# Optimization experiments

Hardware: AMD Instinct MI355X
Metric: run time of the kernel (lower is better)

## Reference

```python
import jax, jax.numpy as jnp
import numpy as np

N, F_IN, H, C, E = 100000, 128, 128, 40, 600000


def setup_inputs() -> dict:
    key = jax.random.key(0)
    ks = jax.random.split(key, 20)
    s = 0.05
    inp = {
        "x": jax.random.normal(ks[0], (N, F_IN), jnp.float32),
        "edge_index": jax.random.randint(ks[1], (2, E), 0, N, jnp.int64),
        "importance": jnp.ones((F_IN,), jnp.float32),
        "W1": jax.random.normal(ks[2], (H, F_IN), jnp.float32) * s,
        "bl1": jax.random.normal(ks[3], (H,), jnp.float32) * s,
        "bc1": jnp.zeros((H,), jnp.float32),
        "W2": jax.random.normal(ks[4], (H, H), jnp.float32) * s,
        "bl2": jax.random.normal(ks[5], (H,), jnp.float32) * s,
        "bc2": jnp.zeros((H,), jnp.float32),
        "W3": jax.random.normal(ks[6], (H, H), jnp.float32) * s,
        "bl3": jax.random.normal(ks[7], (H,), jnp.float32) * s,
        "bc3": jnp.zeros((H,), jnp.float32),
        "Wlin1": jax.random.normal(ks[8], (H, H), jnp.float32) * s,
        "blin1": jax.random.normal(ks[9], (H,), jnp.float32) * s,
        "Wlin2": jax.random.normal(ks[10], (C, H), jnp.float32) * s,
        "blin2": jax.random.normal(ks[11], (C,), jnp.float32) * s,
    }
    return inp


def balanced_conv(x, W, bl, bc, row, col):
    # lin, then symmetric-normalized message, mean-aggregated over targets
    n = x.shape[0]
    h = x @ W.T + bl                                   # [N, H]
    loops = jnp.arange(n)
    r = jnp.concatenate([row, loops])                  # sources (x_j index)
    c = jnp.concatenate([col, loops])                  # targets
    deg = jnp.zeros((n,), x.dtype).at[c].add(1.0)      # degree(col) incl. self-loops
    dinv = deg ** -0.5
    norm = dinv[r] * dinv[c]                           # [E+N]
    msg = norm[:, None] * h[r]                         # gather + scale
    agg = jnp.zeros((n, h.shape[1]), x.dtype).at[c].add(msg)  # scatter-add
    return agg / deg[:, None] + bc                     # mean aggr + bias


def reference(x, edge_index, importance, W1, bl1, bc1, W2, bl2, bc2,
              W3, bl3, bc3, Wlin1, blin1, Wlin2, blin2):
    row, col = edge_index[0], edge_index[1]
    h = x * importance
    h = jax.nn.relu(balanced_conv(h, W1, bl1, bc1, row, col))
    h = jax.nn.relu(balanced_conv(h, W2, bl2, bc2, row, col))
    h = jax.nn.relu(balanced_conv(h, W3, bl3, bc3, row, col))
    h = jax.nn.relu(h @ Wlin1.T + blin1)
    h = h @ Wlin2.T + blin2
    return jax.nn.log_softmax(h, axis=-1)
```

## Files before the change

### kernel.cpp

```cpp
#include <hip/hip_runtime.h>
#include <hip/hip_bf16.h>

#define F 128
#define C_CLS 40
#define NWSPLIT 35
#define ELLCAP 32
#define NBKT 9

typedef __attribute__((ext_vector_type(8))) short short8;
typedef __attribute__((ext_vector_type(4))) float float4v;
typedef unsigned short ushort;

__device__ inline float bf2f(ushort u) {
  unsigned int x = ((unsigned int)u) << 16;
  return __builtin_bit_cast(float, x);
}
__device__ inline ushort f2bf(float f) {
  __hip_bfloat16 h = __float2bfloat16(f);
  return __builtin_bit_cast(ushort, h);
}
__device__ inline void split_bf16(float f, ushort& hi, ushort& lo) {
  hi = f2bf(f);
  lo = f2bf(f - bf2f(hi));
}
__device__ inline int swz(int lane) { return lane ^ ((lane >> 4) & 3); }
__device__ inline int bucket_of(int cv) {
  int lim = cv < ELLCAP ? cv : ELLCAP;
  int nIt = (lim + 3) >> 2;
  return 8 - nIt;
}

__global__ __launch_bounds__(256) void setup_kernel(
    const float* __restrict__ W1, const float* __restrict__ imp,
    const float* __restrict__ W2, const float* __restrict__ W3,
    const float* __restrict__ Wl1, const float* __restrict__ Wh2,
    ushort* __restrict__ WhP,
    ushort* __restrict__ W2hH, ushort* __restrict__ W2lH,
    const int* __restrict__ row, const int* __restrict__ col,
    int* __restrict__ cnt, int* __restrict__ ell,
    int ne, int n) {
  int b = blockIdx.x;
  if (b < NWSPLIT) {
    int ci = b * 256 + threadIdx.x;
    if (ci < 8192) {
      const float* src[4] = {W1, W2, W3, Wl1};
      int p = ci >> 11, c = ci & 2047;
      int kc = c >> 10, ct = (c >> 7) & 7, ks = (c >> 6) & 1, ln = c & 63;
      int dl = swz(ln);
      int colw = ct * 16 + (dl & 15);
      int k = kc * 64 + ks * 32 + (dl >> 4) * 8;
      float4 f0 = *(const float4*)&src[p][(size_t)colw * F + k];
      float4 f1 = *(const float4*)&src[p][(size_t)colw * F + k + 4];
      float v[8] = {f0.x, f0.y, f0.z, f0.w, f1.x, f1.y, f1.z, f1.w};
      if (p == 0) {
        float4 i0 = *(const float4*)&imp[k];
        float4 i1 = *(const float4*)&imp[k + 4];
        v[0] *= i0.x; v[1] *= i0.y; v[2] *= i0.z; v[3] *= i0.w;
        v[4] *= i1.x; v[5] *= i1.y; v[6] *= i1.z; v[7] *= i1.w;
      }
      ushort hi[8];
#pragma unroll
      for (int j = 0; j < 8; ++j) hi[j] = f2bf(v[j]);
      *(short8*)&WhP[(size_t)ci * 8] = *(short8*)hi;
    } else if (ci < 8192 + 768) {
      int c = ci - 8192;
      int ct = c >> 8, ks = (c >> 6) & 3, ln = c & 63;
      int colw = ct * 16 + (ln & 15);
      int k = ks * 32 + (ln >> 4) * 8;
      float v[8];
      if (colw < C_CLS) {
        float4 f0 = *(const float4*)&Wh2[(size_t)colw * F + k];
        float4 f1 = *(const float4*)&Wh2[(size_t)colw * F + k + 4];
        v[0] = f0.x; v[1] = f0.y; v[2] = f0.z; v[3] = f0.w;
        v[4] = f1.x; v[5] = f1.y; v[6] = f1.z; v[7] = f1.w;
      } else {
#pragma unroll
        for (int j = 0; j < 8; ++j) v[j] = 0.f;
      }
      ushort hi[8], lo[8];
#pragma unroll
      for (int j = 0; j < 8; ++j) split_bf16(v[j], hi[j], lo[j]);
      *(short8*)&W2hH[(size_t)c * 8] = *(short8*)hi;
      *(short8*)&W2lH[(size_t)c * 8] = *(short8*)lo;
    }
  } else {
    int e = (b - NWSPLIT) * 256 + threadIdx.x;
    if (e < ne) {
      int r = row[e], c = col[e];
      int p = atomicAdd(&cnt[c], 1);
      if (p < ELLCAP) ell[(size_t)c * ELLCAP + p] = r;
    }
  }
}

__global__ __launch_bounds__(256) void prepass_kernel(
    const float* __restrict__ x, const int* __restrict__ cnt,
    int* __restrict__ ell, float* __restrict__ wsum, int* __restrict__ hist,
    ushort* __restrict__ Xs, ushort* __restrict__ Az,
    int n, int nbW, int nbX) {
  int b = blockIdx.x;
  if (b < nbW) {
    __shared__ int lh[NBKT];
    int t = threadIdx.x;
    if (t < NBKT) lh[t] = 0;
    __syncthreads();
    int node = b * 256 + t;
    if (node < n) {
      int cv = cnt[node];
      int lim = cv < ELLCAP ? cv : ELLCAP;
      int lim4 = (lim + 3) & ~3;
      float gs = 0.f;
      const int4* ep = (const int4*)&ell[(size_t)node * ELLCAP];
      for (int base = 0; base < lim; base += 4) {
        int4 rr = ep[base >> 2];
        bool p1 = base + 1 < lim, p2 = base + 2 < lim, p3 = base + 3 < lim;
        int r1 = p1 ? rr.y : rr.x;
        int r2 = p2 ? rr.z : rr.x;
        int r3 = p3 ? rr.w : rr.x;
        float g0 = rsqrtf((float)(cnt[rr.x] + 1));
        float g1 = p1 ? rsqrtf((float)(cnt[r1] + 1)) : 0.f;
        float g2 = p2 ? rsqrtf((float)(cnt[r2] + 1)) : 0.f;
        float g3 = p3 ? rsqrtf((float)(cnt[r3] + 1)) : 0.f;
        gs += (g0 + g1) + (g2 + g3);
      }
      float d = (float)(cv + 1);
      wsum[node] = rsqrtf(d) * gs + 1.0f / d;
      for (int p = lim; p < lim4; ++p) ell[(size_t)node * ELLCAP + p] = n;
      atomicAdd(&lh[bucket_of(cv)], 1);
    }
    __syncthreads();
    if (t < NBKT) atomicAdd(&hist[t], lh[t]);
  } else if (b < nbW + nbX) {
    size_t i = (size_t)(b - nbW) * 2048 + (size_t)threadIdx.x * 8;
    if (i < (size_t)n * F) {
      int node = (int)(i >> 7);
      float dc = rsqrtf((float)(cnt[node] + 1));
      float4 f0 = *(const float4*)&x[i];
      float4 f1 = *(const float4*)&x[i + 4];
      ushort o[8] = {f2bf(dc * f0.x), f2bf(dc * f0.y), f2bf(dc * f0.z), f2bf(dc * f0.w),
                     f2bf(dc * f1.x), f2bf(dc * f1.y), f2bf(dc * f1.z), f2bf(dc * f1.w)};
      *(short8*)&Xs[i] = *(short8*)o;
    }
  } else {
    int t = threadIdx.x;
    short8 z = (short8){0, 0, 0, 0, 0, 0, 0, 0};
    if (t < 16) *(short8*)&Xs[(size_t)n * F + t * 8] = z;
    else if (t < 32) *(short8*)&Az[(size_t)n * F + (t - 16) * 8] = z;
  }
}

__global__ __launch_bounds__(256) void perm_kernel(
    const int* __restrict__ cnt, const int* __restrict__ hist,
    int* __restrict__ cursor, int* __restrict__ perm, int n) {
  __shared__ int lh[NBKT], lbase[NBKT];
  int t = threadIdx.x;
  if (t < NBKT) lh[t] = 0;
  __syncthreads();
  int node = blockIdx.x * 256 + t;
  int bkt = 0, idx = 0;
  if (node < n) {
    bkt = bucket_of(cnt[node]);
    idx = atomicAdd(&lh[bkt], 1);
  }
  __syncthreads();
  if (t < NBKT) {
    int pre = 0;
#pragma unroll
    for (int k = 0; k < NBKT; ++k)
      if (k < t) pre += hist[k];
    lbase[t] = pre + atomicAdd(&cursor[t], lh[t]);
  }
  __syncthreads();
  if (node < n) perm[lbase[bkt] + idx] = node;
}

template <bool SCALE_OUT>
__global__ __launch_bounds__(256) void conv_fused(
    const int* __restrict__ cnt, const int* __restrict__ ell,
    const int* __restrict__ perm,
    const ushort* __restrict__ Xs, const ushort* __restrict__ Wh,
    const float* __restrict__ wsum, const float* __restrict__ bl,
    const float* __restrict__ bc, ushort* __restrict__ OUT, int n) {
  const int t = threadIdx.x;
  const int w = t >> 6, lane = t & 63, quad = lane >> 4, cl = lane & 15;
  const int gid = blockIdx.x * 64 + w * 16 + cl;
  const bool valid = gid < n;
  const int node = valid ? perm[gid] : 0;

  float acc[4][8];
#pragma unroll
  for (int ks = 0; ks < 4; ++ks)
#pragma unroll
    for (int q = 0; q < 8; ++q) acc[ks][q] = 0.f;

  float dc = 1.f, id = 1.f;
  int nIt = 0;
  if (valid) {
    int cv = cnt[node];
    float d = (float)(cv + 1);
    dc = rsqrtf(d);
    id = 1.0f / d;
    int lim = cv < ELLCAP ? cv : ELLCAP;
    nIt = (lim + 3) >> 2;
  }
  const int4* ep = (const int4*)&ell[(size_t)node * ELLCAP];
  const int qoff = quad * 8;

  if (nIt > 0) {
    int4 rr = ep[0];
    for (int it = 0; it < nIt; ++it) {
      const ushort* r0 = &Xs[(size_t)rr.x * F + qoff];
      const ushort* r1 = &Xs[(size_t)rr.y * F + qoff];
      const ushort* r2 = &Xs[(size_t)rr.z * F + qoff];
      const ushort* r3 = &Xs[(size_t)rr.w * F + qoff];
      short8 v[4][4];
#pragma unroll
      for (int ks = 0; ks < 4; ++ks) {
        v[0][ks] = *(const short8*)&r0[ks * 32];
        v[1][ks] = *(const short8*)&r1[ks * 32];
        v[2][ks] = *(const short8*)&r2[ks * 32];
        v[3][ks] = *(const short8*)&r3[ks * 32];
      }
      int jn = (it + 1 < nIt) ? it + 1 : it;
      rr = ep[jn];
#pragma unroll
      for (int ks = 0; ks < 4; ++ks)
#pragma unroll
        for (int q = 0; q < 8; ++q) {
          float t0 = bf2f((ushort)v[0][ks][q]) + bf2f((ushort)v[1][ks][q]);
          float t1 = bf2f((ushort)v[2][ks][q]) + bf2f((ushort)v[3][ks][q]);
          acc[ks][q] += t0 + t1;
        }
    }
  }

  short8 sfrag[4];
  if (valid) {
    const ushort* sq = &Xs[(size_t)node * F + qoff];
#pragma unroll
    for (int ks = 0; ks < 4; ++ks) {
      short8 sv = *(const short8*)&sq[ks * 32];
      ushort o[8];
#pragma unroll
      for (int q = 0; q < 8; ++q)
        o[q] = f2bf(dc * (acc[ks][q] + bf2f((ushort)sv[q])));
      sfrag[ks] = *(short8*)o;
    }
  } else {
#pragma unroll
    for (int ks = 0; ks < 4; ++ks) sfrag[ks] = (short8){0, 0, 0, 0, 0, 0, 0, 0};
  }

  float4v co[8];
#pragma unroll
  for (int mt = 0; mt < 8; ++mt) co[mt] = (float4v){0.f, 0.f, 0.f, 0.f};
  const int sl = swz(lane);
#pragma unroll
  for (int ks = 0; ks < 4; ++ks) {
    const int base2 = ((ks >> 1) * 1024 + (ks & 1) * 64 + sl) * 8;
#pragma unroll
    for (int mt = 0; mt < 8; ++mt) {
      short8 a_h = *(const short8*)&Wh[base2 + mt * 1024];
      co[mt] = __builtin_amdgcn_mfma_f32_16x16x32_bf16(a_h, sfrag[ks], co[mt], 0, 0, 0);
    }
  }

  if (valid) {
    float ws = wsum[node];
#pragma unroll
    for (int mt = 0; mt < 8; ++mt) {
      float4 blv = *(const float4*)&bl[mt * 16 + quad * 4];
      float4 bcv = *(const float4*)&bc[mt * 16 + quad * 4];
      float v0 = fmaxf((co[mt][0] + ws * blv.x) * id + bcv.x, 0.f);
      float v1 = fmaxf((co[mt][1] + ws * blv.y) * id + bcv.y, 0.f);
      float v2 = fmaxf((co[mt][2] + ws * blv.z) * id + bcv.z, 0.f);
      float v3 = fmaxf((co[mt][3] + ws * blv.w) * id + bcv.w, 0.f);
      if (SCALE_OUT) { v0 *= dc; v1 *= dc; v2 *= dc; v3 *= dc; }
      ushort o[4] = {f2bf(v0), f2bf(v1), f2bf(v2), f2bf(v3)};
      *(ushort4*)&OUT[(size_t)node * F + mt * 16 + quad * 4] = *(ushort4*)o;
    }
  }
}

__global__ __launch_bounds__(256) void head_fused(const ushort* __restrict__ X,
    const ushort* __restrict__ Wl1h, const float* __restrict__ bl,
    const ushort* __restrict__ W2h, const ushort* __restrict__ W2l,
    const float* __restrict__ b2, float* __restrict__ out, int nrows) {
  __shared__ ushort sH[8192];
  __shared__ float b2s[48];
  const int t = threadIdx.x;
  if (t < 48) b2s[t] = (t < C_CLS) ? b2[t] : -1e30f;

  const int w = t >> 6, lane = t & 63;
  const int quad = lane >> 4, cl = lane & 15;
  const int sl = swz(lane);
  const int row0 = (blockIdx.x * 4 + w) * 16;
  char* sHb = (char*)sH;

  float4v acc1[8];
#pragma unroll
  for (int mt = 0; mt < 8; ++mt) acc1[mt] = (float4v){0.f, 0.f, 0.f, 0.f};
  const int gr1 = row0 + cl;
#pragma unroll
  for (int ks = 0; ks < 4; ++ks) {
    short8 b;
    if (gr1 < nrows) b = *(const short8*)&X[(size_t)gr1 * F + ks * 32 + quad * 8];
    else b = (short8){0, 0, 0, 0, 0, 0, 0, 0};
    const int base = ((ks >> 1) * 1024 + (ks & 1) * 64 + sl) * 8;
#pragma unroll
    for (int mt = 0; mt < 8; ++mt) {
      short8 a_h = *(const short8*)&Wl1h[base + mt * 1024];
      acc1[mt] = __builtin_amdgcn_mfma_f32_16x16x32_bf16(a_h, b, acc1[mt], 0, 0, 0);
    }
  }
#pragma unroll
  for (int mt = 0; mt < 8; ++mt) {
    float4 bv = *(const float4*)&bl[mt * 16 + quad * 4];
    ushort o[4];
    o[0] = f2bf(fmaxf(acc1[mt][0] + bv.x, 0.f));
    o[1] = f2bf(fmaxf(acc1[mt][1] + bv.y, 0.f));
    o[2] = f2bf(fmaxf(acc1[mt][2] + bv.z, 0.f));
    o[3] = f2bf(fmaxf(acc1[mt][3] + bv.w, 0.f));
    int ch = (mt * 2 + (quad >> 1)) ^ cl;
    *(ushort4*)&sHb[w * 4096 + cl * 256 + ch * 16 + (quad & 1) * 8] = *(ushort4*)o;
  }
  __syncthreads();

  float4v acc[3];
#pragma unroll
  for (int ct = 0; ct < 3; ++ct) acc[ct] = (float4v){0.f, 0.f, 0.f, 0.f};
#pragma unroll
  for (int ks = 0; ks < 4; ++ks) {
    int ch2 = (ks * 4 + quad) ^ cl;
    short8 a = *(short8*)&sHb[w * 4096 + cl * 256 + ch2 * 16];
#pragma unroll
    for (int ct = 0; ct < 3; ++ct) {
      int chunk = ((ct * 4 + ks) * 64 + lane) * 8;
      short8 b_h = *(const short8*)&W2h[chunk];
      short8 b_l = *(const short8*)&W2l[chunk];
      acc[ct] = __builtin_amdgcn_mfma_f32_16x16x32_bf16(a, b_h, acc[ct], 0, 0, 0);
      acc[ct] = __builtin_amdgcn_mfma_f32_16x16x32_bf16(a, b_l, acc[ct], 0, 0, 0);
    }
  }

  float b0 = b2s[cl], b1 = b2s[16 + cl], b2v = b2s[32 + cl];
  float lse[4];
#pragma unroll
  for (int reg = 0; reg < 4; ++reg) {
    float v0 = acc[0][reg] + b0;
    float v1 = acc[1][reg] + b1;
    float v2 = acc[2][reg] + b2v;
    acc[0][reg] = v0; acc[1][reg] = v1; acc[2][reg] = v2;
    float m = fmaxf(fmaxf(v0, v1), v2);
#pragma unroll
    for (int o = 1; o < 16; o <<= 1) m = fmaxf(m, __shfl_xor(m, o));
    float s = __expf(v0 - m) + __expf(v1 - m) + __expf(v2 - m);
#pragma unroll
    for (int o = 1; o < 16; o <<= 1) s += __shfl_xor(s, o);
    lse[reg] = logf(s) + m;
  }
#pragma unroll
  for (int reg = 0; reg < 4; ++reg) {
    int gr = row0 + quad * 4 + reg;
    if (gr < nrows) {
      out[(size_t)gr * C_CLS + cl] = acc[0][reg] - lse[reg];
      out[(size_t)gr * C_CLS + 16 + cl] = acc[1][reg] - lse[reg];
      if (cl < 8) out[(size_t)gr * C_CLS + 32 + cl] = acc[2][reg] - lse[reg];
    }
  }
}

extern "C" void kernel_launch(void* const* d_in, const int* in_sizes, int n_in,
                              void* d_out, int out_size, void* d_ws, size_t ws_size,
                              hipStream_t stream) {
  const float* x    = (const float*)d_in[0];
  const int*   ei   = (const int*)d_in[1];
  const float* imp  = (const float*)d_in[2];
  const float* W1   = (const float*)d_in[3];
  const float* bl1  = (const float*)d_in[4];
  const float* bc1  = (const float*)d_in[5];
  const float* W2   = (const float*)d_in[6];
  const float* bl2  = (const float*)d_in[7];
  const float* bc2  = (const float*)d_in[8];
  const float* W3   = (const float*)d_in[9];
  const float* bl3  = (const float*)d_in[10];
  const float* bc3  = (const float*)d_in[11];
  const float* Wl1  = (const float*)d_in[12];
  const float* bli1 = (const float*)d_in[13];
  const float* Wl2  = (const float*)d_in[14];
  const float* bli2 = (const float*)d_in[15];
  float* out = (float*)d_out;

  const int N = in_sizes[0] / F;
  const int E = in_sizes[1] / 2;

  ushort* A16 = (ushort*)d_ws;
  ushort* B16 = A16 + (size_t)(N + 1) * F;
  ushort* WhP = B16 + (size_t)(N + 1) * F;
  ushort* W2hH = WhP + 65536;
  ushort* W2lH = W2hH + 6144;
  float* wsum = (float*)(W2lH + 6144);
  int*   cnt  = (int*)(wsum + N);
  int*   hist = cnt + N;
  int*   cursor = hist + NBKT;
  int*   perm = cursor + NBKT;
  int*   ell  = perm + N;

  const int* rowv = ei;
  const int* colv = ei + E;

  int nbE  = (E + 255) / 256;
  int nbW  = (N + 255) / 256;
  int nbX  = (N * F + 2047) / 2048;
  int nbCv = (N + 63) / 64;
  int nbHd = (N + 63) / 64;

  hipMemsetAsync(cnt, 0, ((size_t)N + 2 * NBKT) * sizeof(int), stream);
  setup_kernel<<<NWSPLIT + nbE, 256, 0, stream>>>(
      W1, imp, W2, W3, Wl1, Wl2, WhP, W2hH, W2lH, rowv, colv, cnt, ell, E, N);
  prepass_kernel<<<nbW + nbX + 1, 256, 0, stream>>>(
      x, cnt, ell, wsum, hist, B16, A16, N, nbW, nbX);
  perm_kernel<<<nbW, 256, 0, stream>>>(cnt, hist, cursor, perm, N);

  conv_fused<true ><<<nbCv, 256, 0, stream>>>(cnt, ell, perm, B16, WhP,         wsum, bl1, bc1, A16, N);
  conv_fused<true ><<<nbCv, 256, 0, stream>>>(cnt, ell, perm, A16, WhP + 16384, wsum, bl2, bc2, B16, N);
  conv_fused<false><<<nbCv, 256, 0, stream>>>(cnt, ell, perm, B16, WhP + 32768, wsum, bl3, bc3, A16, N);

  head_fused<<<nbHd, 256, 0, stream>>>(A16, WhP + 49152, bli1, W2hH, W2lH, bli2, out, N);
}
```

Before: 335.7 us.

## Fuse third conv layer with MLP head and make conv kernels persistent

```diff
diff --git a/kernel.cpp b/kernel.cpp
--- a/kernel.cpp
+++ b/kernel.cpp
@@ -174,8 +174,7 @@
   if (node < n) perm[lbase[bkt] + idx] = node;
 }
 
-template <bool SCALE_OUT>
-__global__ __launch_bounds__(256) void conv_fused(
+__global__ __launch_bounds__(256, 5) void conv_fused(
     const int* __restrict__ cnt, const int* __restrict__ ell,
     const int* __restrict__ perm,
     const ushort* __restrict__ Xs, const ushort* __restrict__ Wh,
@@ -183,6 +182,123 @@
     const float* __restrict__ bc, ushort* __restrict__ OUT, int n) {
   const int t = threadIdx.x;
   const int w = t >> 6, lane = t & 63, quad = lane >> 4, cl = lane & 15;
+  const int sl = swz(lane);
+  const int qoff = quad * 8;
+
+  for (int gbase = blockIdx.x * 64; gbase < n; gbase += gridDim.x * 64) {
+    const int gid = gbase + w * 16 + cl;
+    const bool valid = gid < n;
+    const int node = valid ? perm[gid] : 0;
+
+    float acc[4][8];
+#pragma unroll
+    for (int ks = 0; ks < 4; ++ks)
+#pragma unroll
+      for (int q = 0; q < 8; ++q) acc[ks][q] = 0.f;
+
+    float dc = 1.f, id = 1.f;
+    int nIt = 0;
+    if (valid) {
+      int cv = cnt[node];
+      float d = (float)(cv + 1);
+      dc = rsqrtf(d);
+      id = 1.0f / d;
+      int lim = cv < ELLCAP ? cv : ELLCAP;
+      nIt = (lim + 3) >> 2;
+    }
+    const int4* ep = (const int4*)&ell[(size_t)node * ELLCAP];
+
+    if (nIt > 0) {
+      int4 rr = ep[0];
+      for (int it = 0; it < nIt; ++it) {
+        const ushort* r0 = &Xs[(size_t)rr.x * F + qoff];
+        const ushort* r1 = &Xs[(size_t)rr.y * F + qoff];
+        const ushort* r2 = &Xs[(size_t)rr.z * F + qoff];
+        const ushort* r3 = &Xs[(size_t)rr.w * F + qoff];
+        short8 v[4][4];
+#pragma unroll
+        for (int ks = 0; ks < 4; ++ks) {
+          v[0][ks] = *(const short8*)&r0[ks * 32];
+          v[1][ks] = *(const short8*)&r1[ks * 32];
+          v[2][ks] = *(const short8*)&r2[ks * 32];
+          v[3][ks] = *(const short8*)&r3[ks * 32];
+        }
+        int jn = (it + 1 < nIt) ? it + 1 : it;
+        rr = ep[jn];
+#pragma unroll
+        for (int ks = 0; ks < 4; ++ks)
+#pragma unroll
+          for (int q = 0; q < 8; ++q) {
+            float t0 = bf2f((ushort)v[0][ks][q]) + bf2f((ushort)v[1][ks][q]);
+            float t1 = bf2f((ushort)v[2][ks][q]) + bf2f((ushort)v[3][ks][q]);
+            acc[ks][q] += t0 + t1;
+          }
+      }
+    }
+
+    short8 sfrag[4];
+    if (valid) {
+      const ushort* sq = &Xs[(size_t)node * F + qoff];
+#pragma unroll
+      for (int ks = 0; ks < 4; ++ks) {
+        short8 sv = *(const short8*)&sq[ks * 32];
+        ushort o[8];
+#pragma unroll
+        for (int q = 0; q < 8; ++q)
+          o[q] = f2bf(dc * (acc[ks][q] + bf2f((ushort)sv[q])));
+        sfrag[ks] = *(short8*)o;
+      }
+    } else {
+#pragma unroll
+      for (int ks = 0; ks < 4; ++ks) sfrag[ks] = (short8){0, 0, 0, 0, 0, 0, 0, 0};
+    }
+
+    float4v co[8];
+#pragma unroll
+    for (int mt = 0; mt < 8; ++mt) co[mt] = (float4v){0.f, 0.f, 0.f, 0.f};
+#pragma unroll
+    for (int ks = 0; ks < 4; ++ks) {
+      const int base2 = ((ks >> 1) * 1024 + (ks & 1) * 64 + sl) * 8;
+#pragma unroll
+      for (int mt = 0; mt < 8; ++mt) {
+        short8 a_h = *(const short8*)&Wh[base2 + mt * 1024];
+        co[mt] = __builtin_amdgcn_mfma_f32_16x16x32_bf16(a_h, sfrag[ks], co[mt], 0, 0, 0);
+      }
+    }
+
+    if (valid) {
+      float ws = wsum[node];
+#pragma unroll
+      for (int mt = 0; mt < 8; ++mt) {
+        float4 blv = *(const float4*)&bl[mt * 16 + quad * 4];
+        float4 bcv = *(const float4*)&bc[mt * 16 + quad * 4];
+        float v0 = fmaxf((co[mt][0] + ws * blv.x) * id + bcv.x, 0.f) * dc;
+        float v1 = fmaxf((co[mt][1] + ws * blv.y) * id + bcv.y, 0.f) * dc;
+        float v2 = fmaxf((co[mt][2] + ws * blv.z) * id + bcv.z, 0.f) * dc;
+        float v3 = fmaxf((co[mt][3] + ws * blv.w) * id + bcv.w, 0.f) * dc;
+        ushort o[4] = {f2bf(v0), f2bf(v1), f2bf(v2), f2bf(v3)};
+        *(ushort4*)&OUT[(size_t)node * F + mt * 16 + quad * 4] = *(ushort4*)o;
+      }
+    }
+  }
+}
+
+__global__ __launch_bounds__(256) void conv_head(
+    const int* __restrict__ cnt, const int* __restrict__ ell,
+    const int* __restrict__ perm,
+    const ushort* __restrict__ Xs, const ushort* __restrict__ Wh3,
+    const float* __restrict__ wsum, const float* __restrict__ bl3,
+    const float* __restrict__ bc3,
+    const ushort* __restrict__ Wl1h, const float* __restrict__ bli1,
+    const ushort* __restrict__ W2h, const ushort* __restrict__ W2l,
+    const float* __restrict__ b2, float* __restrict__ out, int n) {
+  __shared__ ushort sH[8192];
+  const int t = threadIdx.x;
+  const int w = t >> 6, lane = t & 63, quad = lane >> 4, cl = lane & 15;
+  const int sl = swz(lane);
+  const int qoff = quad * 8;
+  char* sHb = (char*)sH;
+
   const int gid = blockIdx.x * 64 + w * 16 + cl;
   const bool valid = gid < n;
   const int node = valid ? perm[gid] : 0;
@@ -193,18 +309,18 @@
 #pragma unroll
     for (int q = 0; q < 8; ++q) acc[ks][q] = 0.f;
 
-  float dc = 1.f, id = 1.f;
+  float dc = 1.f, id = 1.f, ws = 0.f;
   int nIt = 0;
   if (valid) {
     int cv = cnt[node];
     float d = (float)(cv + 1);
     dc = rsqrtf(d);
     id = 1.0f / d;
+    ws = wsum[node];
     int lim = cv < ELLCAP ? cv : ELLCAP;
     nIt = (lim + 3) >> 2;
   }
   const int4* ep = (const int4*)&ell[(size_t)node * ELLCAP];
-  const int qoff = quad * 8;
 
   if (nIt > 0) {
     int4 rr = ep[0];
@@ -254,68 +370,47 @@
   float4v co[8];
 #pragma unroll
   for (int mt = 0; mt < 8; ++mt) co[mt] = (float4v){0.f, 0.f, 0.f, 0.f};
-  const int sl = swz(lane);
 #pragma unroll
   for (int ks = 0; ks < 4; ++ks) {
     const int base2 = ((ks >> 1) * 1024 + (ks & 1) * 64 + sl) * 8;
 #pragma unroll
     for (int mt = 0; mt < 8; ++mt) {
-      short8 a_h = *(const short8*)&Wh[base2 + mt * 1024];
+      short8 a_h = *(const short8*)&Wh3[base2 + mt * 1024];
       co[mt] = __builtin_amdgcn_mfma_f32_16x16x32_bf16(a_h, sfrag[ks], co[mt], 0, 0, 0);
     }
   }
 
-  if (valid) {
-    float ws = wsum[node];
+#pragma unroll
+  for (int mt = 0; mt < 8; ++mt) {
+    float4 blv = *(const float4*)&bl3[mt * 16 + quad * 4];
+    float4 bcv = *(const float4*)&bc3[mt * 16 + quad * 4];
+    ushort o[4];
+    o[0] = f2bf(fmaxf((co[mt][0] + ws * blv.x) * id + bcv.x, 0.f));
+    o[1] = f2bf(fmaxf((co[mt][1] + ws * blv.y) * id + bcv.y, 0.f));
+    o[2] = f2bf(fmaxf((co[mt][2] + ws * blv.z) * id + bcv.z, 0.f));
+    o[3] = f2bf(fmaxf((co[mt][3] + ws * blv.w) * id + bcv.w, 0.f));
+    int ch = (mt * 2 + (quad >> 1)) ^ cl;
+    *(ushort4*)&sHb[w * 4096 + cl * 256 + ch * 16 + (quad & 1) * 8] = *(ushort4*)o;
+  }
+
+  float4v acc1[8];
+#pragma unroll
+  for (int mt = 0; mt < 8; ++mt) acc1[mt] = (float4v){0.f, 0.f, 0.f, 0.f};
+#pragma unroll
+  for (int ks = 0; ks < 4; ++ks) {
+    int ch2 = (ks * 4 + quad) ^ cl;
+    short8 bfr = *(short8*)&sHb[w * 4096 + cl * 256 + ch2 * 16];
+    const int base2 = ((ks >> 1) * 1024 + (ks & 1) * 64 + sl) * 8;
 #pragma unroll
     for (int mt = 0; mt < 8; ++mt) {
-      float4 blv = *(const float4*)&bl[mt * 16 + quad * 4];
-      float4 bcv = *(const float4*)&bc[mt * 16 + quad * 4];
-      float v0 = fmaxf((co[mt][0] + ws * blv.x) * id + bcv.x, 0.f);
-      float v1 = fmaxf((co[mt][1] + ws * blv.y) * id + bcv.y, 0.f);
-      float v2 = fmaxf((co[mt][2] + ws * blv.z) * id + bcv.z, 0.f);
-      float v3 = fmaxf((co[mt][3] + ws * blv.w) * id + bcv.w, 0.f);
-      if (SCALE_OUT) { v0 *= dc; v1 *= dc; v2 *= dc; v3 *= dc; }
-      ushort o[4] = {f2bf(v0), f2bf(v1), f2bf(v2), f2bf(v3)};
-      *(ushort4*)&OUT[(size_t)node * F + mt * 16 + quad * 4] = *(ushort4*)o;
-    }
-  }
-}
-
-__global__ __launch_bounds__(256) void head_fused(const ushort* __restrict__ X,
-    const ushort* __restrict__ Wl1h, const float* __restrict__ bl,
-    const ushort* __restrict__ W2h, const ushort* __restrict__ W2l,
-    const float* __restrict__ b2, float* __restrict__ out, int nrows) {
-  __shared__ ushort sH[8192];
-  __shared__ float b2s[48];
-  const int t = threadIdx.x;
-  if (t < 48) b2s[t] = (t < C_CLS) ? b2[t] : -1e30f;
-
-  const int w = t >> 6, lane = t & 63;
-  const int quad = lane >> 4, cl = lane & 15;
-  const int sl = swz(lane);
-  const int row0 = (blockIdx.x * 4 + w) * 16;
-  char* sHb = (char*)sH;
-
-  float4v acc1[8];
-#pragma unroll
-  for (int mt = 0; mt < 8; ++mt) acc1[mt] = (float4v){0.f, 0.f, 0.f, 0.f};
-  const int gr1 = row0 + cl;
-#pragma unroll
-  for (int ks = 0; ks < 4; ++ks) {
-    short8 b;
-    if (gr1 < nrows) b = *(const short8*)&X[(size_t)gr1 * F + ks * 32 + quad * 8];
-    else b = (short8){0, 0, 0, 0, 0, 0, 0, 0};
-    const int base = ((ks >> 1) * 1024 + (ks & 1) * 64 + sl) * 8;
-#pragma unroll
-    for (int mt = 0; mt < 8; ++mt) {
-      short8 a_h = *(const short8*)&Wl1h[base + mt * 1024];
-      acc1[mt] = __builtin_amdgcn_mfma_f32_16x16x32_bf16(a_h, b, acc1[mt], 0, 0, 0);
-    }
-  }
+      short8 a_h = *(const short8*)&Wl1h[base2 + mt * 1024];
+      acc1[mt] = __builtin_amdgcn_mfma_f32_16x16x32_bf16(a_h, bfr, acc1[mt], 0, 0, 0);
+    }
+  }
+
 #pragma unroll
   for (int mt = 0; mt < 8; ++mt) {
-    float4 bv = *(const float4*)&bl[mt * 16 + quad * 4];
+    float4 bv = *(const float4*)&bli1[mt * 16 + quad * 4];
     ushort o[4];
     o[0] = f2bf(fmaxf(acc1[mt][0] + bv.x, 0.f));
     o[1] = f2bf(fmaxf(acc1[mt][1] + bv.y, 0.f));
@@ -324,11 +419,10 @@
     int ch = (mt * 2 + (quad >> 1)) ^ cl;
     *(ushort4*)&sHb[w * 4096 + cl * 256 + ch * 16 + (quad & 1) * 8] = *(ushort4*)o;
   }
-  __syncthreads();
-
-  float4v acc[3];
-#pragma unroll
-  for (int ct = 0; ct < 3; ++ct) acc[ct] = (float4v){0.f, 0.f, 0.f, 0.f};
+
+  float4v accl[3];
+#pragma unroll
+  for (int ct = 0; ct < 3; ++ct) accl[ct] = (float4v){0.f, 0.f, 0.f, 0.f};
 #pragma unroll
   for (int ks = 0; ks < 4; ++ks) {
     int ch2 = (ks * 4 + quad) ^ cl;
@@ -338,19 +432,21 @@
       int chunk = ((ct * 4 + ks) * 64 + lane) * 8;
       short8 b_h = *(const short8*)&W2h[chunk];
       short8 b_l = *(const short8*)&W2l[chunk];
-      acc[ct] = __builtin_amdgcn_mfma_f32_16x16x32_bf16(a, b_h, acc[ct], 0, 0, 0);
-      acc[ct] = __builtin_amdgcn_mfma_f32_16x16x32_bf16(a, b_l, acc[ct], 0, 0, 0);
-    }
-  }
-
-  float b0 = b2s[cl], b1 = b2s[16 + cl], b2v = b2s[32 + cl];
+      accl[ct] = __builtin_amdgcn_mfma_f32_16x16x32_bf16(a, b_h, accl[ct], 0, 0, 0);
+      accl[ct] = __builtin_amdgcn_mfma_f32_16x16x32_bf16(a, b_l, accl[ct], 0, 0, 0);
+    }
+  }
+
+  float b0 = b2[cl];
+  float b1 = b2[16 + cl];
+  float b2v = (32 + cl < C_CLS) ? b2[32 + cl] : -1e30f;
   float lse[4];
 #pragma unroll
   for (int reg = 0; reg < 4; ++reg) {
-    float v0 = acc[0][reg] + b0;
-    float v1 = acc[1][reg] + b1;
-    float v2 = acc[2][reg] + b2v;
-    acc[0][reg] = v0; acc[1][reg] = v1; acc[2][reg] = v2;
+    float v0 = accl[0][reg] + b0;
+    float v1 = accl[1][reg] + b1;
+    float v2 = accl[2][reg] + b2v;
+    accl[0][reg] = v0; accl[1][reg] = v1; accl[2][reg] = v2;
     float m = fmaxf(fmaxf(v0, v1), v2);
 #pragma unroll
     for (int o = 1; o < 16; o <<= 1) m = fmaxf(m, __shfl_xor(m, o));
@@ -359,13 +455,15 @@
     for (int o = 1; o < 16; o <<= 1) s += __shfl_xor(s, o);
     lse[reg] = logf(s) + m;
   }
+  int vn = valid ? node : -1;
 #pragma unroll
   for (int reg = 0; reg < 4; ++reg) {
-    int gr = row0 + quad * 4 + reg;
-    if (gr < nrows) {
-      out[(size_t)gr * C_CLS + cl] = acc[0][reg] - lse[reg];
-      out[(size_t)gr * C_CLS + 16 + cl] = acc[1][reg] - lse[reg];
-      if (cl < 8) out[(size_t)gr * C_CLS + 32 + cl] = acc[2][reg] - lse[reg];
+    int s = quad * 4 + reg;
+    int gn = __shfl(vn, s);
+    if (gn >= 0) {
+      out[(size_t)gn * C_CLS + cl] = accl[0][reg] - lse[reg];
+      out[(size_t)gn * C_CLS + 16 + cl] = accl[1][reg] - lse[reg];
+      if (cl < 8) out[(size_t)gn * C_CLS + 32 + cl] = accl[2][reg] - lse[reg];
     }
   }
 }
@@ -413,7 +511,7 @@
   int nbW  = (N + 255) / 256;
   int nbX  = (N * F + 2047) / 2048;
   int nbCv = (N + 63) / 64;
-  int nbHd = (N + 63) / 64;
+  int nbP  = nbCv < 1280 ? nbCv : 1280;
 
   hipMemsetAsync(cnt, 0, ((size_t)N + 2 * NBKT) * sizeof(int), stream);
   setup_kernel<<<NWSPLIT + nbE, 256, 0, stream>>>(
@@ -422,9 +520,9 @@
       x, cnt, ell, wsum, hist, B16, A16, N, nbW, nbX);
   perm_kernel<<<nbW, 256, 0, stream>>>(cnt, hist, cursor, perm, N);
 
-  conv_fused<true ><<<nbCv, 256, 0, stream>>>(cnt, ell, perm, B16, WhP,         wsum, bl1, bc1, A16, N);
-  conv_fused<true ><<<nbCv, 256, 0, stream>>>(cnt, ell, perm, A16, WhP + 16384, wsum, bl2, bc2, B16, N);
-  conv_fused<false><<<nbCv, 256, 0, stream>>>(cnt, ell, perm, B16, WhP + 32768, wsum, bl3, bc3, A16, N);
-
-  head_fused<<<nbHd, 256, 0, stream>>>(A16, WhP + 49152, bli1, W2hH, W2lH, bli2, out, N);
-}
+  conv_fused<<<nbP, 256, 0, stream>>>(cnt, ell, perm, B16, WhP,         wsum, bl1, bc1, A16, N);
+  conv_fused<<<nbP, 256, 0, stream>>>(cnt, ell, perm, A16, WhP + 16384, wsum, bl2, bc2, B16, N);
+
+  conv_head<<<nbCv, 256, 0, stream>>>(cnt, ell, perm, B16, WhP + 32768, wsum, bl3, bc3,
+                                      WhP + 49152, bli1, W2hH, W2lH, bli2, out, N);
+}
```

After: 570.9 us. 1.7x slower.
